# Performance work log

Hardware: AMD Instinct MI355X
Metric: run time of the kernel (lower is better)

The kernel has to match this reference:

```python
import jax, jax.numpy as jnp
import numpy as np

B, T, H = 4, 8192, 512
LN_EPS = 1e-5


def _ln(x, g, b):
    mu = jnp.mean(x, axis=-1, keepdims=True)
    var = jnp.mean((x - mu) ** 2, axis=-1, keepdims=True)
    return (x - mu) * jax.lax.rsqrt(var + LN_EPS) * g + b


def _log_g(x):
    # log of g(x) = x + 0.5 (x >= 0) else sigmoid(x); both branches NaN-safe.
    return jnp.where(x >= 0, jnp.log(jax.nn.relu(x) + 0.5), -jax.nn.softplus(-x))


def _min_gru(x, Wz, bz, Wh, bh):
    # minGRU parallel log-space scan ("Were RNNs All We Needed?" Alg.), h_0 = 0.
    k = x @ Wz + bz                      # [B,T,H] gate pre-activation
    log_z = -jax.nn.softplus(-k)         # log sigmoid(k)
    log_coeffs = -jax.nn.softplus(k)     # log (1 - sigmoid(k))
    log_tilde_h = _log_g(x @ Wh + bh)
    log_h0 = jnp.full((x.shape[0], 1, x.shape[2]), jnp.log(0.5), x.dtype)  # g(0)=0.5
    log_values = jnp.concatenate([log_h0, log_z + log_tilde_h], axis=1)   # [B,T+1,H]
    a_star = jnp.cumsum(jnp.pad(log_coeffs, ((0, 0), (1, 0), (0, 0))), axis=1)
    log_h = a_star + jax.lax.cumlogsumexp(log_values - a_star, axis=1)
    return jnp.exp(log_h)[:, 1:]         # drop h_0 slot -> [B,T,H]


def setup_inputs() -> dict:
    key = jax.random.key(0)
    ks = jax.random.split(key, 5)
    s = 1.0 / np.sqrt(H)
    return {
        "x": jax.random.normal(ks[0], (B, T, H), jnp.float32),
        "ln1_g": jnp.ones((H,), jnp.float32),
        "ln1_b": jnp.zeros((H,), jnp.float32),
        "Wz": jax.random.normal(ks[1], (H, H), jnp.float32) * s,
        "bz": jnp.zeros((H,), jnp.float32),
        "Wh": jax.random.normal(ks[2], (H, H), jnp.float32) * s,
        "bh": jnp.zeros((H,), jnp.float32),
        "ln2_g": jnp.ones((H,), jnp.float32),
        "ln2_b": jnp.zeros((H,), jnp.float32),
        "W1": jax.random.normal(ks[3], (H, H), jnp.float32) * s,
        "b1": jnp.zeros((H,), jnp.float32),
        "W2": jax.random.normal(ks[4], (H, H), jnp.float32) * s,
        "b2": jnp.zeros((H,), jnp.float32),
    }


def reference(x, ln1_g, ln1_b, Wz, bz, Wh, bh, ln2_g, ln2_b, W1, b1, W2, b2):
    # x = x + minGRU(ln_1(x))   (dropout=0 -> identity)
    x = x + _min_gru(_ln(x, ln1_g, ln1_b), Wz, bz, Wh, bh)
    # x = x + FFN(ln_2(x)) ; FFN = Linear -> ReLU -> Linear (hidden->hidden)
    h = jax.nn.relu(_ln(x, ln2_g, ln2_b) @ W1 + b1)
    x = x + (h @ W2 + b2)
    return x
```

## Files before the change

kernel.cpp:

```cpp
#include <hip/hip_runtime.h>

typedef unsigned short u16;
typedef unsigned int u32;
typedef __bf16 bf16x8 __attribute__((ext_vector_type(8)));
typedef float f32x4 __attribute__((ext_vector_type(4)));
typedef u16 u16x8 __attribute__((ext_vector_type(8)));

__device__ __forceinline__ u16 f2bf(float f) {
    union { float f; u32 i; } v; v.f = f;
    u32 x = v.i;
    u32 r = (x + 0x7fffu + ((x >> 16) & 1u)) >> 16;
    return (u16)r;
}
__device__ __forceinline__ float bf2f(u16 u) {
    union { u32 i; float f; } v; v.i = ((u32)u) << 16; return v.f;
}
__device__ __forceinline__ u16 f2h(float f) {
    union { _Float16 h; u16 u; } v; v.h = (_Float16)f; return v.u;
}
__device__ __forceinline__ float h2f(u16 u) {
    union { _Float16 h; u16 u; } v; v.u = u; return (float)v.h;
}

__device__ __forceinline__ void gld16(const void* g, void* l) {
    __builtin_amdgcn_global_load_lds(
        (const __attribute__((address_space(1))) void*)g,
        (__attribute__((address_space(3))) void*)l, 16, 0, 0);
}

__global__ __launch_bounds__(256) void transpose4(
    const float* __restrict__ s0, const float* __restrict__ s1,
    const float* __restrict__ s2, const float* __restrict__ s3,
    u16* __restrict__ d0, u16* __restrict__ d1,
    u16* __restrict__ d2, u16* __restrict__ d3)
{
    int bx = blockIdx.x;
    int mat = bx >> 8;
    int tile = bx & 255;
    int tx = (tile & 15) * 32;
    int ty = (tile >> 4) * 32;
    const float* src = (mat == 0) ? s0 : (mat == 1) ? s1 : (mat == 2) ? s2 : s3;
    u16* dst = (mat == 0) ? d0 : (mat == 1) ? d1 : (mat == 2) ? d2 : d3;

    __shared__ u16 tl[32][33];
    int col = threadIdx.x & 31;
    int r8  = threadIdx.x >> 5;
    #pragma unroll
    for (int k = 0; k < 4; ++k) {
        int rr = r8 + k * 8;
        tl[rr][col] = f2bf(src[(ty + rr) * 512 + tx + col]);
    }
    __syncthreads();
    #pragma unroll
    for (int k = 0; k < 4; ++k) {
        int rr = r8 + k * 8;
        dst[(tx + rr) * 512 + ty + col] = tl[col][rr];
    }
}

__global__ __launch_bounds__(256) void ln_k(
    const float* __restrict__ x, const float* __restrict__ g,
    const float* __restrict__ b, u16* __restrict__ y, int rows)
{
    int gid = blockIdx.x * blockDim.x + threadIdx.x;
    int row = gid >> 6;
    int lane = gid & 63;
    if (row >= rows) return;

    const float* xr = x + (size_t)row * 512 + lane * 8;
    float4 a0 = *(const float4*)xr;
    float4 a1 = *(const float4*)(xr + 4);
    float f[8] = {a0.x, a0.y, a0.z, a0.w, a1.x, a1.y, a1.z, a1.w};
    float s = 0.f, s2 = 0.f;
    #pragma unroll
    for (int e = 0; e < 8; ++e) { s += f[e]; s2 += f[e] * f[e]; }
    #pragma unroll
    for (int o = 32; o > 0; o >>= 1) { s += __shfl_xor(s, o); s2 += __shfl_xor(s2, o); }
    const float inv = 1.0f / 512.0f;
    float mean = s * inv;
    float var  = s2 * inv - mean * mean;
    float rstd = rsqrtf(var + 1e-5f);

    float4 g0 = *(const float4*)(g + lane * 8);
    float4 g1 = *(const float4*)(g + lane * 8 + 4);
    float4 b0 = *(const float4*)(b + lane * 8);
    float4 b1 = *(const float4*)(b + lane * 8 + 4);
    float gg[8] = {g0.x, g0.y, g0.z, g0.w, g1.x, g1.y, g1.z, g1.w};
    float bb[8] = {b0.x, b0.y, b0.z, b0.w, b1.x, b1.y, b1.z, b1.w};
    u16x8 ov;
    #pragma unroll
    for (int e = 0; e < 8; ++e)
        ov[e] = f2bf((f[e] - mean) * rstd * gg[e] + bb[e]);
    *(u16x8*)(y + (size_t)row * 512 + lane * 8) = ov;
}

template <int MODE>
__global__ __launch_bounds__(256, 2) void gemm_bt(
    const u16* __restrict__ A, const u16* __restrict__ Bt0,
    const u16* __restrict__ Bt1, const float* __restrict__ bias0,
    const float* __restrict__ bias1, const float* __restrict__ resid,
    void* __restrict__ out0v, u16* __restrict__ out1,
    float* __restrict__ chCp, float* __restrict__ chVp)
{
    constexpr int Kd = 512, Nd = 512;
    constexpr int SMEM_N = (MODE == 0) ? 12288 : 8192;
    __shared__ __align__(16) u16 smem[SMEM_N];
    u16* As  = smem;
    u16* Bs0 = smem + 4096;
    u16* Bs1 = smem + 8192;

    int bx = blockIdx.x;
    bx = (bx & 7) * 128 + (bx >> 3);
    int m0 = (bx >> 2) * 128;
    int n0 = (bx & 3) * 128;
    int tid = threadIdx.x;
    int lane = tid & 63;
    int w = tid >> 6;
    int wm = w & 1, wn = w >> 1;
    int l16 = lane & 15;
    int quad = lane >> 4;

    f32x4 acc0[4][4] = {};
    f32x4 acc1[4][4] = {};

    int ch0 = tid, ch1 = tid + 256;
    int row0 = ch0 >> 2, row1 = ch1 >> 2;
    int g0 = (ch0 & 3) ^ ((ch0 >> 3) & 3);
    int g1 = (ch1 & 3) ^ ((ch1 >> 3) & 3);
    const u16* a0p  = A   + (size_t)(m0 + row0) * Kd + g0 * 8;
    const u16* a1p  = A   + (size_t)(m0 + row1) * Kd + g1 * 8;
    const u16* b00p = Bt0 + (size_t)(n0 + row0) * Kd + g0 * 8;
    const u16* b01p = Bt0 + (size_t)(n0 + row1) * Kd + g1 * 8;
    const u16* b10p = (MODE == 0) ? Bt1 + (size_t)(n0 + row0) * Kd + g0 * 8 : nullptr;
    const u16* b11p = (MODE == 0) ? Bt1 + (size_t)(n0 + row1) * Kd + g1 * 8 : nullptr;

    for (int kt = 0; kt < Kd / 32; ++kt) {
        int k0 = kt * 32;
        gld16(a0p  + k0, &As [ch0 * 8]);
        gld16(a1p  + k0, &As [ch1 * 8]);
        gld16(b00p + k0, &Bs0[ch0 * 8]);
        gld16(b01p + k0, &Bs0[ch1 * 8]);
        if (MODE == 0) {
            gld16(b10p + k0, &Bs1[ch0 * 8]);
            gld16(b11p + k0, &Bs1[ch1 * 8]);
        }
        __syncthreads();

        bf16x8 af[4], bf0[4], bf1[4];
        #pragma unroll
        for (int i = 0; i < 4; ++i) {
            int ra = wm * 64 + i * 16 + l16;
            int rb = wn * 64 + i * 16 + l16;
            int ga = quad ^ ((ra >> 1) & 3);
            int gb = quad ^ ((rb >> 1) & 3);
            af[i]  = *(const bf16x8*)&As [ra * 32 + ga * 8];
            bf0[i] = *(const bf16x8*)&Bs0[rb * 32 + gb * 8];
            if (MODE == 0)
                bf1[i] = *(const bf16x8*)&Bs1[rb * 32 + gb * 8];
        }
        #pragma unroll
        for (int i = 0; i < 4; ++i)
            #pragma unroll
            for (int j = 0; j < 4; ++j) {
                acc0[i][j] = __builtin_amdgcn_mfma_f32_16x16x32_bf16(af[i], bf0[j], acc0[i][j], 0, 0, 0);
                if (MODE == 0)
                    acc1[i][j] = __builtin_amdgcn_mfma_f32_16x16x32_bf16(af[i], bf1[j], acc1[i][j], 0, 0, 0);
            }
        __syncthreads();
    }

    if (MODE == 0) {
        u16* cb = (u16*)out0v;
        #pragma unroll
        for (int p = 0; p < 2; ++p) {
            int grow = m0 + wm * 64 + p * 32;
            int bb_  = grow >> 13;
            int chgl = (grow & 8191) >> 5;
            #pragma unroll
            for (int j = 0; j < 4; ++j) {
                int col = n0 + wn * 64 + j * 16 + l16;
                float bk  = bias0[col];
                float bh2 = bias1[col];
                float Cs[2], Vs[2];
                #pragma unroll
                for (int ii = 0; ii < 2; ++ii) {
                    int i = 2 * p + ii;
                    float C = 1.f, V = 0.f;
                    #pragma unroll
                    for (int r = 0; r < 4; ++r) {
                        int row = m0 + wm * 64 + i * 16 + quad * 4 + r;
                        float kk = acc0[i][j][r] + bk;
                        float hh = acc1[i][j][r] + bh2;
                        float z = __builtin_amdgcn_rcpf(1.f + __expf(-kk));
                        float c = 1.f - z;
                        float gs = __builtin_amdgcn_rcpf(1.f + __expf(-hh));
                        float gg = (hh >= 0.f) ? (hh + 0.5f) : gs;
                        float v = z * gg;
                        size_t off = (size_t)row * Nd + col;
                        cb[off]   = f2h(c);
                        out1[off] = f2h(v);
                        C *= c;
                        V = fmaf(c, V, v);
                    }
                    Cs[ii] = C; Vs[ii] = V;
                }
                #pragma unroll
                for (int ii = 0; ii < 2; ++ii) {
                    float C = Cs[ii], V = Vs[ii];
                    float oc = __shfl_xor(C, 16), ov = __shfl_xor(V, 16);
                    V = (quad & 1) ? fmaf(C, ov, V) : fmaf(oc, V, ov);
                    C *= oc;
                    oc = __shfl_xor(C, 32); ov = __shfl_xor(V, 32);
                    V = (quad & 2) ? fmaf(C, ov, V) : fmaf(oc, V, ov);
                    C *= oc;
                    Cs[ii] = C; Vs[ii] = V;
                }
                float Cch = Cs[0] * Cs[1];
                float Vch = fmaf(Cs[1], Vs[0], Vs[1]);
                if (quad == 0) {
                    int idx = chgl * 2048 + bb_ * 512 + col;
                    chCp[idx] = Cch;
                    chVp[idx] = Vch;
                }
            }
        }
    } else {
        #pragma unroll
        for (int j = 0; j < 4; ++j) {
            int col = n0 + wn * 64 + j * 16 + l16;
            float b0 = bias0[col];
            #pragma unroll
            for (int i = 0; i < 4; ++i) {
                #pragma unroll
                for (int r = 0; r < 4; ++r) {
                    int row = m0 + wm * 64 + i * 16 + quad * 4 + r;
                    size_t off = (size_t)row * Nd + col;
                    float v0 = acc0[i][j][r] + b0;
                    if (MODE == 1) {
                        ((u16*)out0v)[off] = f2bf(fmaxf(v0, 0.f));
                    } else {
                        ((float*)out0v)[off] = v0 + resid[off];
                    }
                }
            }
        }
    }
}


__global__ __launch_bounds__(256) void scanB1(
    const float* __restrict__ chC, const float* __restrict__ chV,
    float* __restrict__ scC, float* __restrict__ scV)
{
    int gid = blockIdx.x * 256 + threadIdx.x;
    int s = gid & 2047;
    int sc = gid >> 11;
    float C = 1.f, V = 0.f;
    #pragma unroll 4
    for (int i = 0; i < 16; ++i) {
        int ch = sc * 16 + i;
        float c = chC[ch * 2048 + s];
        float v = chV[ch * 2048 + s];
        C *= c;
        V = fmaf(c, V, v);
    }
    scC[sc * 2048 + s] = C;
    scV[sc * 2048 + s] = V;
}

__global__ __launch_bounds__(256) void scanB2(
    const float* __restrict__ scC, const float* __restrict__ scV,
    float* __restrict__ sst)
{
    int s = blockIdx.x * 256 + threadIdx.x;
    float hcur = 0.5f;
    #pragma unroll
    for (int sc = 0; sc < 16; ++sc) {
        sst[sc * 2048 + s] = hcur;
        hcur = fmaf(scC[sc * 2048 + s], hcur, scV[sc * 2048 + s]);
    }
}

__global__ __launch_bounds__(256) void scanB3(
    const float* __restrict__ chC, const float* __restrict__ chV,
    const float* __restrict__ sst, float* __restrict__ hst)
{
    int gid = blockIdx.x * 256 + threadIdx.x;
    int s = gid & 2047;
    int sc = gid >> 11;
    float hcur = sst[sc * 2048 + s];
    #pragma unroll 4
    for (int i = 0; i < 16; ++i) {
        int ch = sc * 16 + i;
        hst[ch * 2048 + s] = hcur;
        hcur = fmaf(chC[ch * 2048 + s], hcur, chV[ch * 2048 + s]);
    }
}

__global__ __launch_bounds__(256) void scanC(
    const u16* __restrict__ cb, const u16* __restrict__ vb,
    const float* __restrict__ hst, const float* __restrict__ x,
    float* __restrict__ x2)
{
    int gid = blockIdx.x * 256 + threadIdx.x;
    int h = gid & 511;
    int rest = gid >> 9;
    int b = rest & 3;
    int ch = rest >> 2;
    size_t base = ((size_t)(b * 8192 + ch * 32)) * 512 + h;
    float hcur = hst[ch * 2048 + b * 512 + h];
    #pragma unroll 8
    for (int t = 0; t < 32; ++t) {
        size_t off = base + (size_t)t * 512;
        float c = h2f(cb[off]);
        float v = h2f(vb[off]);
        hcur = fmaf(c, hcur, v);
        x2[off] = x[off] + hcur;
    }
}

extern "C" void kernel_launch(void* const* d_in, const int* in_sizes, int n_in,
                              void* d_out, int out_size, void* d_ws, size_t ws_size,
                              hipStream_t stream)
{
    const float* x    = (const float*)d_in[0];
    const float* ln1g = (const float*)d_in[1];
    const float* ln1b = (const float*)d_in[2];
    const float* Wz   = (const float*)d_in[3];
    const float* bz   = (const float*)d_in[4];
    const float* Wh   = (const float*)d_in[5];
    const float* bh   = (const float*)d_in[6];
    const float* ln2g = (const float*)d_in[7];
    const float* ln2b = (const float*)d_in[8];
    const float* W1   = (const float*)d_in[9];
    const float* b1   = (const float*)d_in[10];
    const float* W2   = (const float*)d_in[11];
    const float* b2   = (const float*)d_in[12];
    float* out = (float*)d_out;

    char* ws = (char*)d_ws;
    constexpr size_t MB = 1024 * 1024;
    u16* Wzt = (u16*)(ws);
    u16* Wht = Wzt + 262144;
    u16* W1t = Wzt + 524288;
    u16* W2t = Wzt + 786432;
    u16* a  = (u16*)(ws + 3 * MB + 512 * 1024);
    u16* cb = (u16*)(ws + 35 * MB + 512 * 1024);
    u16* vb = (u16*)(ws + 67 * MB + 512 * 1024);
    float* hst = (float*)(ws + 3 * MB + 512 * 1024);
    float* scC = hst + 524288;
    float* scV = scC + 32768;
    float* sst = scV + 32768;
    float* chC = (float*)d_out;
    float* chV = chC + 524288;

    transpose4<<<1024, 256, 0, stream>>>(Wz, Wh, W1, W2, Wzt, Wht, W1t, W2t);
    ln_k<<<8192, 256, 0, stream>>>(x, ln1g, ln1b, a, 32768);
    gemm_bt<0><<<1024, 256, 0, stream>>>(a, Wzt, Wht, bz, bh, nullptr, cb, vb, chC, chV);
    scanB1<<<128, 256, 0, stream>>>(chC, chV, scC, scV);
    scanB2<<<8, 256, 0, stream>>>(scC, scV, sst);
    scanB3<<<128, 256, 0, stream>>>(chC, chV, sst, hst);
    scanC<<<2048, 256, 0, stream>>>(cb, vb, hst, x, out);
    ln_k<<<8192, 256, 0, stream>>>(out, ln2g, ln2b, a, 32768);
    gemm_bt<1><<<1024, 256, 0, stream>>>(a, W1t, nullptr, b1, nullptr, nullptr, cb, nullptr, nullptr, nullptr);
    gemm_bt<2><<<1024, 256, 0, stream>>>(cb, W2t, nullptr, b2, nullptr, out, out, nullptr, nullptr, nullptr);
}
```

Before: 304.0 us.

## Double-buffer GEMM shared-memory tiles and interleave gate/value fp16 pairs

The GEMM k-loop now uses two shared-memory buffers and issues the next tile's global-to-LDS loads before computing on the current tile. This removes one barrier per iteration and lets memory latency overlap with MFMA work. The first-stage epilogue now packs the coefficient and value fp16 pair into one 32-bit word, and scanC processes two columns per thread with vector loads and stores, halving its grid. Doubling LDS (up to 48KB for mode 0) may lower occupancy under the launch bounds of 2 blocks per SM.

```diff
diff --git a/kernel.cpp b/kernel.cpp
--- a/kernel.cpp
+++ b/kernel.cpp
@@ -99,15 +99,12 @@
     const u16* __restrict__ A, const u16* __restrict__ Bt0,
     const u16* __restrict__ Bt1, const float* __restrict__ bias0,
     const float* __restrict__ bias1, const float* __restrict__ resid,
-    void* __restrict__ out0v, u16* __restrict__ out1,
+    void* __restrict__ out0v,
     float* __restrict__ chCp, float* __restrict__ chVp)
 {
     constexpr int Kd = 512, Nd = 512;
-    constexpr int SMEM_N = (MODE == 0) ? 12288 : 8192;
-    __shared__ __align__(16) u16 smem[SMEM_N];
-    u16* As  = smem;
-    u16* Bs0 = smem + 4096;
-    u16* Bs1 = smem + 8192;
+    constexpr int BUF = (MODE == 0) ? 12288 : 8192;
+    __shared__ __align__(16) u16 smem[2 * BUF];
 
     int bx = blockIdx.x;
     bx = (bx & 7) * 128 + (bx >> 3);
@@ -134,18 +131,28 @@
     const u16* b10p = (MODE == 0) ? Bt1 + (size_t)(n0 + row0) * Kd + g0 * 8 : nullptr;
     const u16* b11p = (MODE == 0) ? Bt1 + (size_t)(n0 + row1) * Kd + g1 * 8 : nullptr;
 
+#define STAGE(sl, kt) { \
+    int k0_ = (kt) * 32; \
+    u16* As_ = smem + (sl) * BUF; \
+    gld16(a0p  + k0_, &As_[ch0 * 8]); \
+    gld16(a1p  + k0_, &As_[ch1 * 8]); \
+    gld16(b00p + k0_, &As_[4096 + ch0 * 8]); \
+    gld16(b01p + k0_, &As_[4096 + ch1 * 8]); \
+    if (MODE == 0) { \
+        gld16(b10p + k0_, &As_[8192 + ch0 * 8]); \
+        gld16(b11p + k0_, &As_[8192 + ch1 * 8]); \
+    } }
+
+    STAGE(0, 0);
+    __syncthreads();
+
     for (int kt = 0; kt < Kd / 32; ++kt) {
-        int k0 = kt * 32;
-        gld16(a0p  + k0, &As [ch0 * 8]);
-        gld16(a1p  + k0, &As [ch1 * 8]);
-        gld16(b00p + k0, &Bs0[ch0 * 8]);
-        gld16(b01p + k0, &Bs0[ch1 * 8]);
-        if (MODE == 0) {
-            gld16(b10p + k0, &Bs1[ch0 * 8]);
-            gld16(b11p + k0, &Bs1[ch1 * 8]);
-        }
-        __syncthreads();
-
+        int cur = kt & 1;
+        if (kt < Kd / 32 - 1) STAGE(cur ^ 1, kt + 1);
+
+        const u16* As  = smem + cur * BUF;
+        const u16* Bs0 = As + 4096;
+        const u16* Bs1 = As + 8192;
         bf16x8 af[4], bf0[4], bf1[4];
         #pragma unroll
         for (int i = 0; i < 4; ++i) {
@@ -168,9 +175,10 @@
             }
         __syncthreads();
     }
+#undef STAGE
 
     if (MODE == 0) {
-        u16* cb = (u16*)out0v;
+        u32* cvb = (u32*)out0v;
         #pragma unroll
         for (int p = 0; p < 2; ++p) {
             int grow = m0 + wm * 64 + p * 32;
@@ -196,9 +204,8 @@
                         float gs = __builtin_amdgcn_rcpf(1.f + __expf(-hh));
                         float gg = (hh >= 0.f) ? (hh + 0.5f) : gs;
                         float v = z * gg;
-                        size_t off = (size_t)row * Nd + col;
-                        cb[off]   = f2h(c);
-                        out1[off] = f2h(v);
+                        cvb[(size_t)row * Nd + col] =
+                            (u32)f2h(c) | ((u32)f2h(v) << 16);
                         C *= c;
                         V = fmaf(c, V, v);
                     }
@@ -298,24 +305,26 @@
 }
 
 __global__ __launch_bounds__(256) void scanC(
-    const u16* __restrict__ cb, const u16* __restrict__ vb,
-    const float* __restrict__ hst, const float* __restrict__ x,
-    float* __restrict__ x2)
+    const u32* __restrict__ cv, const float* __restrict__ hst,
+    const float* __restrict__ x, float* __restrict__ x2)
 {
     int gid = blockIdx.x * 256 + threadIdx.x;
-    int h = gid & 511;
-    int rest = gid >> 9;
+    int h2 = (gid & 255) * 2;
+    int rest = gid >> 8;
     int b = rest & 3;
     int ch = rest >> 2;
-    size_t base = ((size_t)(b * 8192 + ch * 32)) * 512 + h;
-    float hcur = hst[ch * 2048 + b * 512 + h];
+    size_t base = ((size_t)(b * 8192 + ch * 32)) * 512 + h2;
+    int sidx = ch * 2048 + b * 512 + h2;
+    float h0 = hst[sidx], h1 = hst[sidx + 1];
     #pragma unroll 8
     for (int t = 0; t < 32; ++t) {
         size_t off = base + (size_t)t * 512;
-        float c = h2f(cb[off]);
-        float v = h2f(vb[off]);
-        hcur = fmaf(c, hcur, v);
-        x2[off] = x[off] + hcur;
+        uint2 g2 = *(const uint2*)(cv + off);
+        float2 xx = *(const float2*)(x + off);
+        h0 = fmaf(h2f((u16)(g2.x & 0xffffu)), h0, h2f((u16)(g2.x >> 16)));
+        h1 = fmaf(h2f((u16)(g2.y & 0xffffu)), h1, h2f((u16)(g2.y >> 16)));
+        float2 o; o.x = xx.x + h0; o.y = xx.y + h1;
+        *(float2*)(x2 + off) = o;
     }
 }
 
@@ -344,9 +353,9 @@
     u16* Wht = Wzt + 262144;
     u16* W1t = Wzt + 524288;
     u16* W2t = Wzt + 786432;
-    u16* a  = (u16*)(ws + 3 * MB + 512 * 1024);
-    u16* cb = (u16*)(ws + 35 * MB + 512 * 1024);
-    u16* vb = (u16*)(ws + 67 * MB + 512 * 1024);
+    u16* a   = (u16*)(ws + 3 * MB + 512 * 1024);
+    u32* cv  = (u32*)(ws + 35 * MB + 512 * 1024);
+    u16* hid = (u16*)(ws + 35 * MB + 512 * 1024);
     float* hst = (float*)(ws + 3 * MB + 512 * 1024);
     float* scC = hst + 524288;
     float* scV = scC + 32768;
@@ -356,12 +365,12 @@
 
     transpose4<<<1024, 256, 0, stream>>>(Wz, Wh, W1, W2, Wzt, Wht, W1t, W2t);
     ln_k<<<8192, 256, 0, stream>>>(x, ln1g, ln1b, a, 32768);
-    gemm_bt<0><<<1024, 256, 0, stream>>>(a, Wzt, Wht, bz, bh, nullptr, cb, vb, chC, chV);
+    gemm_bt<0><<<1024, 256, 0, stream>>>(a, Wzt, Wht, bz, bh, nullptr, cv, chC, chV);
     scanB1<<<128, 256, 0, stream>>>(chC, chV, scC, scV);
     scanB2<<<8, 256, 0, stream>>>(scC, scV, sst);
     scanB3<<<128, 256, 0, stream>>>(chC, chV, sst, hst);
-    scanC<<<2048, 256, 0, stream>>>(cb, vb, hst, x, out);
+    scanC<<<1024, 256, 0, stream>>>(cv, hst, x, out);
     ln_k<<<8192, 256, 0, stream>>>(out, ln2g, ln2b, a, 32768);
-    gemm_bt<1><<<1024, 256, 0, stream>>>(a, W1t, nullptr, b1, nullptr, nullptr, cb, nullptr, nullptr, nullptr);
-    gemm_bt<2><<<1024, 256, 0, stream>>>(cb, W2t, nullptr, b2, nullptr, out, out, nullptr, nullptr, nullptr);
-}
+    gemm_bt<1><<<1024, 256, 0, stream>>>(a, W1t, nullptr, b1, nullptr, nullptr, hid, nullptr, nullptr);
+    gemm_bt<2><<<1024, 256, 0, stream>>>(hid, W2t, nullptr, b2, nullptr, out, out, nullptr, nullptr);
+}
```

Result: faster. 296.2 us (-2.6%).
